# Performance work log

Hardware: AMD Instinct MI355X
Metric: run time of the kernel (lower is better)

Reference implementation:

```python
import jax, jax.numpy as jnp
import numpy as np

B, C_IN, W, H = 16, 512, 40, 40
HC = 64  # hide_channel


def setup_inputs() -> dict:
    key = jax.random.key(0)
    ks = jax.random.split(key, 6)
    def xavier(k, shape):
        fan_in, fan_out = shape
        lim = np.sqrt(6.0 / (fan_in + fan_out))
        return jax.random.uniform(k, shape, jnp.float32, -lim, lim)
    return {
        "rgb": jax.random.normal(ks[0], (B, C_IN, W, H), jnp.float32),
        "hsi": jax.random.normal(ks[1], (B, C_IN, W, H), jnp.float32),
        "wq": xavier(ks[2], (C_IN, HC)),
        "wk": xavier(ks[3], (C_IN, HC)),
        "wv": xavier(ks[4], (C_IN, HC)),
        "wo": xavier(ks[5], (HC, C_IN)),
    }


def reference(rgb, hsi, wq, wk, wv, wo):
    b, c, w, h = rgb.shape
    n = w * h
    # [B, C, W, H] -> [B, N, C] tokens
    x0 = jnp.swapaxes(rgb.reshape(b, c, n), 1, 2)
    x1 = jnp.swapaxes(hsi.reshape(b, c, n), 1, 2)
    q = x0 @ wq              # [B, N, HC]
    k = x0 @ wk              # [B, N, HC]
    v = x1 @ wv              # [B, N, HC]
    hc = q.shape[-1]
    scale = hc ** (-0.5)
    attn = jax.nn.softmax(jnp.einsum('bnd,bmd->bnm', q, k) * scale, axis=-1)  # [B, N, N]
    res = jnp.einsum('bnm,bmd->bnd', attn, v)  # [B, N, HC]
    # Faithful to torch: .transpose(1, 2).reshape(B, N, HC) (layout reinterpretation)
    res = jnp.swapaxes(res, 1, 2).reshape(b, n, hc)
    out = res @ wo                              # [B, N, C]
    out = jnp.swapaxes(out, 1, 2).reshape(b, c, w, h)
    return out
```

## Files before the change

### kernel.cpp

```cpp
#include <hip/hip_runtime.h>
#include <cstddef>

#define NB   16
#define CIN  512
#define NTOK 1600
#define HCH  64
#define LDA  72

typedef __attribute__((ext_vector_type(8))) short bf16x8;
typedef __attribute__((ext_vector_type(4))) float f32x4;

__device__ __forceinline__ unsigned short f2bf(float x) {
    union { float f; unsigned u; } v; v.f = x;
    unsigned r = v.u + 0x7FFFu + ((v.u >> 16) & 1u);
    return (unsigned short)(r >> 16);
}

__device__ __forceinline__ unsigned cvtpk_bf16(float lo, float hi) {
    unsigned r;
    asm("v_cvt_pk_bf16_f32 %0, %1, %2" : "=v"(r) : "v"(lo), "v"(hi));
    return r;
}

__device__ __forceinline__ float fast_exp2(float x) {
#if __has_builtin(__builtin_amdgcn_exp2f)
    return __builtin_amdgcn_exp2f(x);
#else
    return exp2f(x);
#endif
}

__global__ void __launch_bounds__(256) wprep_kernel(
    const float* __restrict__ wq, const float* __restrict__ wk,
    const float* __restrict__ wv, const float* __restrict__ wo,
    unsigned short* __restrict__ Wt, unsigned short* __restrict__ WoT)
{
    const int gid = blockIdx.x * 256 + threadIdx.x;
    if (gid < 3 * HCH * (CIN / 8)) {
        const int h  = gid & 63;
        const int c8 = (gid >> 6) & 63;
        const int t  = gid >> 12;
        const float* w = (t == 0) ? wq : (t == 1) ? wk : wv;
        ushort4 lo, hi;
        lo.x = f2bf(w[(size_t)(c8 * 8 + 0) * HCH + h]);
        lo.y = f2bf(w[(size_t)(c8 * 8 + 1) * HCH + h]);
        lo.z = f2bf(w[(size_t)(c8 * 8 + 2) * HCH + h]);
        lo.w = f2bf(w[(size_t)(c8 * 8 + 3) * HCH + h]);
        hi.x = f2bf(w[(size_t)(c8 * 8 + 4) * HCH + h]);
        hi.y = f2bf(w[(size_t)(c8 * 8 + 5) * HCH + h]);
        hi.z = f2bf(w[(size_t)(c8 * 8 + 6) * HCH + h]);
        hi.w = f2bf(w[(size_t)(c8 * 8 + 7) * HCH + h]);
        ushort4* dst = (ushort4*)(Wt + ((size_t)t * HCH + h) * CIN + c8 * 8);
        dst[0] = lo; dst[1] = hi;
    } else {
        const int g  = gid - 3 * HCH * (CIN / 8);
        const int c  = g & 511;
        const int j8 = g >> 9;
        ushort4 lo, hi;
        lo.x = f2bf(wo[(size_t)(j8 * 8 + 0) * CIN + c]);
        lo.y = f2bf(wo[(size_t)(j8 * 8 + 1) * CIN + c]);
        lo.z = f2bf(wo[(size_t)(j8 * 8 + 2) * CIN + c]);
        lo.w = f2bf(wo[(size_t)(j8 * 8 + 3) * CIN + c]);
        hi.x = f2bf(wo[(size_t)(j8 * 8 + 4) * CIN + c]);
        hi.y = f2bf(wo[(size_t)(j8 * 8 + 5) * CIN + c]);
        hi.z = f2bf(wo[(size_t)(j8 * 8 + 6) * CIN + c]);
        hi.w = f2bf(wo[(size_t)(j8 * 8 + 7) * CIN + c]);
        ushort4* dst = (ushort4*)(WoT + (size_t)c * HCH + j8 * 8);
        dst[0] = lo; dst[1] = hi;
    }
}

__global__ void __launch_bounds__(256) proj_kernel(
    const float* __restrict__ rgb, const float* __restrict__ hsi,
    const unsigned short* __restrict__ Wt,
    unsigned short* __restrict__ Q, unsigned short* __restrict__ K,
    unsigned short* __restrict__ Vt)
{
    __shared__ __align__(16) unsigned short As[64 * LDA];
    __shared__ __align__(16) unsigned short Ws[128 * LDA];

    const int which = blockIdx.y;
    const int b    = blockIdx.x / 25;
    const int n0   = (blockIdx.x % 25) * 64;
    const int tid  = threadIdx.x;
    const int wv_  = tid >> 6;
    const int lane = tid & 63;
    const int l16  = lane & 15, quad = lane >> 4;

    const float* __restrict__ src = which ? hsi : rgb;
    const unsigned short* __restrict__ wbase = Wt + (which ? (size_t)2 * HCH * CIN : 0);
    const int nW = which ? 1 : 2;

    f32x4 acc[2][4];
    #pragma unroll
    for (int t = 0; t < 2; ++t)
        #pragma unroll
        for (int nt = 0; nt < 4; ++nt)
            #pragma unroll
            for (int r = 0; r < 4; ++r) acc[t][nt][r] = 0.f;

    const int cc = tid >> 2;
    const int nq = tid & 3;
    const int swz = cc >> 3;
    const int clo = cc & 7;
    const int swzr = (l16 >> 1) & 6;

    for (int c0 = 0; c0 < CIN; c0 += 64) {
        __syncthreads();
        {
            const float* gs = src + ((size_t)b * CIN + c0 + cc) * NTOK + n0;
            #pragma unroll
            for (int rep = 0; rep < 4; ++rep) {
                const int nn4 = rep * 4 + nq;
                const float4 a = ((const float4*)gs)[nn4];
                const int n = nn4 * 4;
                const int i01 = ((swz ^ ((n >> 1) & 6)) << 3) + clo;
                const int i23 = ((swz ^ (((n + 2) >> 1) & 6)) << 3) + clo;
                As[(n + 0) * LDA + i01] = f2bf(a.x);
                As[(n + 1) * LDA + i01] = f2bf(a.y);
                As[(n + 2) * LDA + i23] = f2bf(a.z);
                As[(n + 3) * LDA + i23] = f2bf(a.w);
            }
        }
        for (int task = tid; task < nW * 512; task += 256) {
            const int row = task >> 3, ch = task & 7;
            *((int4*)(Ws + row * LDA + ch * 8)) =
                *((const int4*)(wbase + (size_t)row * CIN + c0 + ch * 8));
        }
        __syncthreads();

        #pragma unroll
        for (int k0 = 0; k0 < 2; ++k0) {
            const bf16x8 av = *((const bf16x8*)(As + (wv_ * 16 + l16) * LDA + ((k0 * 4 + quad) ^ swzr) * 8));
            if (which == 0) {
                #pragma unroll
                for (int t = 0; t < 2; ++t)
                    #pragma unroll
                    for (int nt = 0; nt < 4; ++nt) {
                        const bf16x8 bv = *((const bf16x8*)(Ws + (t * 64 + nt * 16 + l16) * LDA + k0 * 32 + quad * 8));
                        acc[t][nt] = __builtin_amdgcn_mfma_f32_16x16x32_bf16(av, bv, acc[t][nt], 0, 0, 0);
                    }
            } else {
                #pragma unroll
                for (int nt = 0; nt < 4; ++nt) {
                    const bf16x8 bv = *((const bf16x8*)(Ws + (nt * 16 + l16) * LDA + k0 * 32 + quad * 8));
                    acc[0][nt] = __builtin_amdgcn_mfma_f32_16x16x32_bf16(av, bv, acc[0][nt], 0, 0, 0);
                }
            }
        }
    }

    if (which == 0) {
        const float qscale = 0.18033688f;
        #pragma unroll
        for (int nt = 0; nt < 4; ++nt) {
            const int h = nt * 16 + l16;
            #pragma unroll
            for (int r = 0; r < 4; ++r) {
                const int n = n0 + wv_ * 16 + quad * 4 + r;
                Q[((size_t)b * NTOK + n) * HCH + h] = f2bf(acc[0][nt][r] * qscale);
                K[((size_t)b * NTOK + n) * HCH + h] = f2bf(acc[1][nt][r]);
            }
        }
    } else {
        const int pbase = n0 + (wv_ & 1) * 32 + quad * 8 + (wv_ >> 1) * 4;
        #pragma unroll
        for (int nt = 0; nt < 4; ++nt) {
            const int h = nt * 16 + l16;
            ushort4 pv;
            pv.x = f2bf(acc[0][nt][0]); pv.y = f2bf(acc[0][nt][1]);
            pv.z = f2bf(acc[0][nt][2]); pv.w = f2bf(acc[0][nt][3]);
            *((ushort4*)(Vt + ((size_t)b * HCH + h) * NTOK + pbase)) = pv;
        }
    }
}

__device__ __forceinline__ void attn_stage_tile(
    const unsigned short* __restrict__ Kg, const unsigned short* __restrict__ Vg,
    char* buf, int kt, int wv_, int srow, int scole)
{
    #pragma unroll
    for (int i = 0; i < 2; ++i) {
        const int ck  = i * 4 + wv_;
        const int row = ck * 8 + srow;
        const unsigned short* ksrc = Kg + (size_t)(kt * 64 + row) * HCH + scole;
        __builtin_amdgcn_global_load_lds(ksrc, buf + ck * 1024, 16, 0, 0);
        const unsigned short* vsrc = Vg + (size_t)row * NTOK + kt * 64 + scole;
        __builtin_amdgcn_global_load_lds(vsrc, buf + 8192 + ck * 1024, 16, 0, 0);
    }
}

__device__ __forceinline__ void attn_compute_lds(
    const char* kbuf, const char* vbuf, int l16, int quad,
    const bf16x8 (&qa)[2], f32x4 (&o)[4], float& rs)
{
    bf16x8 kb[2][4], vb[2][4];
    #pragma unroll
    for (int k0 = 0; k0 < 2; ++k0) {
        const int colb = (k0 * 64 + quad * 16) ^ ((l16 & 7) << 4);
        #pragma unroll
        for (int nt = 0; nt < 4; ++nt) {
            kb[k0][nt] = *((const bf16x8*)(kbuf + (nt * 16 + l16) * 128 + colb));
            vb[k0][nt] = *((const bf16x8*)(vbuf + (nt * 16 + l16) * 128 + colb));
        }
    }

    f32x4 s[4];
    #pragma unroll
    for (int nt = 0; nt < 4; ++nt)
        #pragma unroll
        for (int r = 0; r < 4; ++r) s[nt][r] = 0.f;
    #pragma unroll
    for (int k0 = 0; k0 < 2; ++k0)
        #pragma unroll
        for (int nt = 0; nt < 4; ++nt)
            s[nt] = __builtin_amdgcn_mfma_f32_16x16x32_bf16(kb[k0][nt], qa[k0], s[nt], 0, 0, 0);

    unsigned dA[4], dB[4];
    #pragma unroll
    for (int nt = 0; nt < 4; ++nt) {
        const float e0 = fast_exp2(s[nt][0]);
        const float e1 = fast_exp2(s[nt][1]);
        const float e2 = fast_exp2(s[nt][2]);
        const float e3 = fast_exp2(s[nt][3]);
        rs += (e0 + e1) + (e2 + e3);
        dA[nt] = cvtpk_bf16(e0, e1);
        dB[nt] = cvtpk_bf16(e2, e3);
    }

    #pragma unroll
    for (int k0 = 0; k0 < 2; ++k0) {
        union { bf16x8 v; unsigned u[4]; } pu;
        pu.u[0] = dA[k0];
        pu.u[1] = dB[k0];
        pu.u[2] = dA[k0 + 2];
        pu.u[3] = dB[k0 + 2];
        #pragma unroll
        for (int nt = 0; nt < 4; ++nt)
            o[nt] = __builtin_amdgcn_mfma_f32_16x16x32_bf16(pu.v, vb[k0][nt], o[nt], 0, 0, 0);
    }
}

__global__ void __launch_bounds__(256) attn_kernel(
    const unsigned short* __restrict__ Q, const unsigned short* __restrict__ K,
    const unsigned short* __restrict__ Vt, unsigned short* __restrict__ Rt2)
{
    __shared__ __align__(16) char sbuf[2][16384];

    const int bx   = blockIdx.x;
    const int b    = 2 * (bx & 7) + (((bx >> 3) >= 25) ? 1 : 0);
    const int qt   = (bx >> 3) % 25;
    const int tid  = threadIdx.x;
    const int wv_  = tid >> 6;
    const int lane = tid & 63;
    const int l16  = lane & 15, quad = lane >> 4;

    const unsigned short* Qg = Q  + ((size_t)b * NTOK + qt * 64 + wv_ * 16) * HCH;
    const unsigned short* Kg = K  + (size_t)b * NTOK * HCH;
    const unsigned short* Vg = Vt + (size_t)b * HCH * NTOK;

    const int srow  = lane >> 3;
    const int scole = 8 * ((lane & 7) ^ srow);

    bf16x8 qa[2];
    #pragma unroll
    for (int k0 = 0; k0 < 2; ++k0)
        qa[k0] = *((const bf16x8*)(Qg + (size_t)l16 * HCH + k0 * 32 + quad * 8));

    f32x4 o[4];
    float rs = 0.f;
    #pragma unroll
    for (int nt = 0; nt < 4; ++nt)
        #pragma unroll
        for (int r = 0; r < 4; ++r) o[nt][r] = 0.f;

    attn_stage_tile(Kg, Vg, sbuf[0], 0, wv_, srow, scole);
    int cur = 0;
    for (int kt = 0; kt < 25; ++kt) {
        if (kt + 1 < 25) {
            attn_stage_tile(Kg, Vg, sbuf[cur ^ 1], kt + 1, wv_, srow, scole);
            asm volatile("s_waitcnt vmcnt(4)" ::: "memory");
        } else {
            asm volatile("s_waitcnt vmcnt(0)" ::: "memory");
        }
        __builtin_amdgcn_sched_barrier(0);
        __builtin_amdgcn_s_barrier();
        __builtin_amdgcn_sched_barrier(0);
        attn_compute_lds(sbuf[cur], sbuf[cur] + 8192, l16, quad, qa, o, rs);
        __builtin_amdgcn_sched_barrier(0);
        __builtin_amdgcn_s_barrier();
        cur ^= 1;
    }

    rs += __shfl_xor(rs, 16);
    rs += __shfl_xor(rs, 32);
    float rsq[4];
    #pragma unroll
    for (int r = 0; r < 4; ++r) rsq[r] = __shfl(rs, quad * 4 + r);

    unsigned short* Rg = Rt2 + ((size_t)(b * 25 + qt)) * HCH * HCH;
    #pragma unroll
    for (int nt = 0; nt < 4; ++nt) {
        ushort4 pk;
        pk.x = f2bf(o[nt][0] / rsq[0]);
        pk.y = f2bf(o[nt][1] / rsq[1]);
        pk.z = f2bf(o[nt][2] / rsq[2]);
        pk.w = f2bf(o[nt][3] / rsq[3]);
        *((ushort4*)(Rg + (size_t)(nt * 16 + l16) * HCH + wv_ * 16 + quad * 4)) = pk;
    }
}

__global__ void __launch_bounds__(256) outproj_kernel(
    const unsigned short* __restrict__ Rt2, const unsigned short* __restrict__ WoT,
    float* __restrict__ out)
{
    __shared__ __align__(16) unsigned short Aw[64 * LDA];

    const int b    = blockIdx.x;
    const int ct   = blockIdx.y;
    const int nt64 = blockIdx.z;
    const int tid  = threadIdx.x;
    const int wv_  = tid >> 6;
    const int lane = tid & 63;
    const int l16  = lane & 15, quad = lane >> 4;

    #pragma unroll
    for (int r = 0; r < 2; ++r) {
        const int task = tid + r * 256;
        const int row = task >> 3, ch = task & 7;
        *((int4*)(Aw + row * LDA + ch * 8)) =
            *((const int4*)(WoT + ((size_t)(ct * 64 + row)) * HCH + ch * 8));
    }
    __syncthreads();

    const int n = nt64 * 64 + wv_ * 16 + l16;
    const int h = n / 25, t = n % 25;
    const unsigned short* bsrc = Rt2 + ((size_t)(b * 25 + t) * HCH + h) * HCH;

    f32x4 acc[4];
    #pragma unroll
    for (int mt = 0; mt < 4; ++mt)
        #pragma unroll
        for (int r = 0; r < 4; ++r) acc[mt][r] = 0.f;

    #pragma unroll
    for (int k0 = 0; k0 < 2; ++k0) {
        const bf16x8 bv = *((const bf16x8*)(bsrc + k0 * 32 + quad * 8));
        #pragma unroll
        for (int mt = 0; mt < 4; ++mt) {
            const bf16x8 av = *((const bf16x8*)(Aw + (mt * 16 + l16) * LDA + k0 * 32 + quad * 8));
            acc[mt] = __builtin_amdgcn_mfma_f32_16x16x32_bf16(av, bv, acc[mt], 0, 0, 0);
        }
    }
    #pragma unroll
    for (int mt = 0; mt < 4; ++mt)
        #pragma unroll
        for (int r = 0; r < 4; ++r)
            out[((size_t)b * CIN + ct * 64 + mt * 16 + quad * 4 + r) * NTOK + n] = acc[mt][r];
}

extern "C" void kernel_launch(void* const* d_in, const int* in_sizes, int n_in,
                              void* d_out, int out_size, void* d_ws, size_t ws_size,
                              hipStream_t stream)
{
    const float* rgb = (const float*)d_in[0];
    const float* hsi = (const float*)d_in[1];
    const float* wq  = (const float*)d_in[2];
    const float* wk  = (const float*)d_in[3];
    const float* wv  = (const float*)d_in[4];
    const float* wo  = (const float*)d_in[5];
    float* out = (float*)d_out;

    unsigned short* Wt  = (unsigned short*)d_ws;
    unsigned short* WoT = Wt  + (size_t)3 * HCH * CIN;
    unsigned short* Qb  = WoT + (size_t)CIN * HCH;
    unsigned short* Kb  = Qb  + (size_t)NB * NTOK * HCH;
    unsigned short* Vtb = Kb  + (size_t)NB * NTOK * HCH;
    unsigned short* Rt2 = Vtb + (size_t)NB * NTOK * HCH;

    wprep_kernel<<<dim3(64), 256, 0, stream>>>(wq, wk, wv, wo, Wt, WoT);
    proj_kernel<<<dim3(NB * 25, 2), 256, 0, stream>>>(rgb, hsi, Wt, Qb, Kb, Vtb);
    attn_kernel<<<dim3(NB * 25), 256, 0, stream>>>(Qb, Kb, Vtb, Rt2);
    outproj_kernel<<<dim3(NB, 8, 25), 256, 0, stream>>>(Rt2, WoT, out);
}
```

Baseline: 184.6 us.

## Double-buffer projection kernel with async LDS weight DMA and register prefetch

The projection GEMM now double-buffers its activation and weight LDS tiles. The next fp32 input chunk is prefetched into registers, and weights are loaded directly into LDS with global_load_lds using an XOR swizzle. Hand-placed waitcnt and barrier calls overlap these loads with MFMA compute on the current chunk, replacing the old load-sync-compute loop. Templating on the weight count removes the runtime branch, at the cost of doubled LDS use and fragile manual vmcnt accounting.

```diff
diff --git a/kernel.cpp b/kernel.cpp
--- a/kernel.cpp
+++ b/kernel.cpp
@@ -70,87 +70,134 @@
     }
 }
 
-__global__ void __launch_bounds__(256) proj_kernel(
-    const float* __restrict__ rgb, const float* __restrict__ hsi,
-    const unsigned short* __restrict__ Wt,
+__device__ __forceinline__ void proj_load_in(
+    const float* __restrict__ gsb, int c0, int nq, float4 (&inr)[4])
+{
+    #pragma unroll
+    for (int rep = 0; rep < 4; ++rep)
+        inr[rep] = ((const float4*)(gsb + (size_t)c0 * NTOK))[rep * 4 + nq];
+}
+
+__device__ __forceinline__ void proj_write_as(
+    unsigned short* Ab, const float4 (&inr)[4], int nq, int swz, int clo)
+{
+    #pragma unroll
+    for (int rep = 0; rep < 4; ++rep) {
+        const int nn4 = rep * 4 + nq;
+        const float4 a = inr[rep];
+        const int n = nn4 * 4;
+        const int i01 = ((swz ^ ((n >> 1) & 6)) << 3) + clo;
+        const int i23 = ((swz ^ (((n + 2) >> 1) & 6)) << 3) + clo;
+        Ab[(n + 0) * LDA + i01] = f2bf(a.x);
+        Ab[(n + 1) * LDA + i01] = f2bf(a.y);
+        Ab[(n + 2) * LDA + i23] = f2bf(a.z);
+        Ab[(n + 3) * LDA + i23] = f2bf(a.w);
+    }
+}
+
+template<int NW>
+__device__ __forceinline__ void proj_dma_w(
+    const unsigned short* __restrict__ wbase, int c0,
+    unsigned short* Wb, int wv_, int lane)
+{
+    const int sr = lane >> 3;
+    const int sc = 8 * ((lane & 7) ^ sr);
+    #pragma unroll
+    for (int r = 0; r < 2 * NW; ++r) {
+        const int row0 = r * 32 + wv_ * 8;
+        __builtin_amdgcn_global_load_lds(
+            wbase + (size_t)(row0 + sr) * CIN + c0 + sc,
+            (char*)Wb + row0 * 128, 16, 0, 0);
+    }
+}
+
+template<int NW>
+__device__ __forceinline__ void proj_compute(
+    const unsigned short* Ab, const unsigned short* Wb,
+    int wv_, int l16, int quad, int swzr, f32x4 (&acc)[NW][4])
+{
+    #pragma unroll
+    for (int k0 = 0; k0 < 2; ++k0) {
+        const bf16x8 av = *((const bf16x8*)(Ab + (wv_ * 16 + l16) * LDA + ((k0 * 4 + quad) ^ swzr) * 8));
+        const int colb = (k0 * 64 + quad * 16) ^ ((l16 & 7) << 4);
+        #pragma unroll
+        for (int t = 0; t < NW; ++t)
+            #pragma unroll
+            for (int nt = 0; nt < 4; ++nt) {
+                const bf16x8 bv = *((const bf16x8*)((const char*)Wb + (t * 64 + nt * 16 + l16) * 128 + colb));
+                acc[t][nt] = __builtin_amdgcn_mfma_f32_16x16x32_bf16(av, bv, acc[t][nt], 0, 0, 0);
+            }
+    }
+}
+
+template<int NW>
+__device__ __forceinline__ void proj_body(
+    const float* __restrict__ src, const unsigned short* __restrict__ wbase,
     unsigned short* __restrict__ Q, unsigned short* __restrict__ K,
-    unsigned short* __restrict__ Vt)
-{
-    __shared__ __align__(16) unsigned short As[64 * LDA];
-    __shared__ __align__(16) unsigned short Ws[128 * LDA];
-
-    const int which = blockIdx.y;
-    const int b    = blockIdx.x / 25;
-    const int n0   = (blockIdx.x % 25) * 64;
-    const int tid  = threadIdx.x;
+    unsigned short* __restrict__ Vt,
+    unsigned short* As, unsigned short* Wl, int b, int n0, int tid)
+{
     const int wv_  = tid >> 6;
     const int lane = tid & 63;
     const int l16  = lane & 15, quad = lane >> 4;
-
-    const float* __restrict__ src = which ? hsi : rgb;
-    const unsigned short* __restrict__ wbase = Wt + (which ? (size_t)2 * HCH * CIN : 0);
-    const int nW = which ? 1 : 2;
-
-    f32x4 acc[2][4];
-    #pragma unroll
-    for (int t = 0; t < 2; ++t)
+    const int cc   = tid >> 2, nq = tid & 3;
+    const int swz  = cc >> 3,  clo = cc & 7;
+    const int swzr = (l16 >> 1) & 6;
+
+    f32x4 acc[NW][4];
+    #pragma unroll
+    for (int t = 0; t < NW; ++t)
         #pragma unroll
         for (int nt = 0; nt < 4; ++nt)
             #pragma unroll
             for (int r = 0; r < 4; ++r) acc[t][nt][r] = 0.f;
 
-    const int cc = tid >> 2;
-    const int nq = tid & 3;
-    const int swz = cc >> 3;
-    const int clo = cc & 7;
-    const int swzr = (l16 >> 1) & 6;
-
-    for (int c0 = 0; c0 < CIN; c0 += 64) {
-        __syncthreads();
-        {
-            const float* gs = src + ((size_t)b * CIN + c0 + cc) * NTOK + n0;
-            #pragma unroll
-            for (int rep = 0; rep < 4; ++rep) {
-                const int nn4 = rep * 4 + nq;
-                const float4 a = ((const float4*)gs)[nn4];
-                const int n = nn4 * 4;
-                const int i01 = ((swz ^ ((n >> 1) & 6)) << 3) + clo;
-                const int i23 = ((swz ^ (((n + 2) >> 1) & 6)) << 3) + clo;
-                As[(n + 0) * LDA + i01] = f2bf(a.x);
-                As[(n + 1) * LDA + i01] = f2bf(a.y);
-                As[(n + 2) * LDA + i23] = f2bf(a.z);
-                As[(n + 3) * LDA + i23] = f2bf(a.w);
+    const float* gsb = src + ((size_t)b * CIN + cc) * NTOK + n0;
+
+    float4 inr[4];
+    proj_load_in(gsb, 0, nq, inr);
+    __builtin_amdgcn_sched_barrier(0);
+    proj_dma_w<NW>(wbase, 0, Wl, wv_, lane);
+    if constexpr (NW == 2) asm volatile("s_waitcnt vmcnt(4)" ::: "memory");
+    else                   asm volatile("s_waitcnt vmcnt(2)" ::: "memory");
+    __builtin_amdgcn_sched_barrier(0);
+    proj_write_as(As, inr, nq, swz, clo);
+    proj_load_in(gsb, 64, nq, inr);
+    __builtin_amdgcn_sched_barrier(0);
+    proj_dma_w<NW>(wbase, 64, Wl + 128 * 64, wv_, lane);
+    if constexpr (NW == 2) asm volatile("s_waitcnt vmcnt(8) lgkmcnt(0)" ::: "memory");
+    else                   asm volatile("s_waitcnt vmcnt(6) lgkmcnt(0)" ::: "memory");
+    __builtin_amdgcn_sched_barrier(0);
+    __builtin_amdgcn_s_barrier();
+    __builtin_amdgcn_sched_barrier(0);
+
+    for (int t = 0; t < 8; ++t) {
+        proj_compute<NW>(As + (t & 1) * (64 * LDA), Wl + (t & 1) * (128 * 64),
+                         wv_, l16, quad, swzr, acc);
+        __builtin_amdgcn_sched_barrier(0);
+        __builtin_amdgcn_s_barrier();
+        __builtin_amdgcn_sched_barrier(0);
+        if (t < 7) {
+            if constexpr (NW == 2) asm volatile("s_waitcnt vmcnt(4)" ::: "memory");
+            else                   asm volatile("s_waitcnt vmcnt(2)" ::: "memory");
+            __builtin_amdgcn_sched_barrier(0);
+            proj_write_as(As + ((t + 1) & 1) * (64 * LDA), inr, nq, swz, clo);
+            if (t < 6) {
+                proj_load_in(gsb, (t + 2) * 64, nq, inr);
+                __builtin_amdgcn_sched_barrier(0);
+                proj_dma_w<NW>(wbase, (t + 2) * 64, Wl + (t & 1) * (128 * 64), wv_, lane);
+                if constexpr (NW == 2) asm volatile("s_waitcnt vmcnt(8) lgkmcnt(0)" ::: "memory");
+                else                   asm volatile("s_waitcnt vmcnt(6) lgkmcnt(0)" ::: "memory");
+            } else {
+                asm volatile("s_waitcnt vmcnt(0) lgkmcnt(0)" ::: "memory");
             }
-        }
-        for (int task = tid; task < nW * 512; task += 256) {
-            const int row = task >> 3, ch = task & 7;
-            *((int4*)(Ws + row * LDA + ch * 8)) =
-                *((const int4*)(wbase + (size_t)row * CIN + c0 + ch * 8));
-        }
-        __syncthreads();
-
-        #pragma unroll
-        for (int k0 = 0; k0 < 2; ++k0) {
-            const bf16x8 av = *((const bf16x8*)(As + (wv_ * 16 + l16) * LDA + ((k0 * 4 + quad) ^ swzr) * 8));
-            if (which == 0) {
-                #pragma unroll
-                for (int t = 0; t < 2; ++t)
-                    #pragma unroll
-                    for (int nt = 0; nt < 4; ++nt) {
-                        const bf16x8 bv = *((const bf16x8*)(Ws + (t * 64 + nt * 16 + l16) * LDA + k0 * 32 + quad * 8));
-                        acc[t][nt] = __builtin_amdgcn_mfma_f32_16x16x32_bf16(av, bv, acc[t][nt], 0, 0, 0);
-                    }
-            } else {
-                #pragma unroll
-                for (int nt = 0; nt < 4; ++nt) {
-                    const bf16x8 bv = *((const bf16x8*)(Ws + (nt * 16 + l16) * LDA + k0 * 32 + quad * 8));
-                    acc[0][nt] = __builtin_amdgcn_mfma_f32_16x16x32_bf16(av, bv, acc[0][nt], 0, 0, 0);
-                }
-            }
-        }
-    }
-
-    if (which == 0) {
+            __builtin_amdgcn_sched_barrier(0);
+            __builtin_amdgcn_s_barrier();
+            __builtin_amdgcn_sched_barrier(0);
+        }
+    }
+
+    if constexpr (NW == 2) {
         const float qscale = 0.18033688f;
         #pragma unroll
         for (int nt = 0; nt < 4; ++nt) {
@@ -175,6 +222,26 @@
     }
 }
 
+__global__ void __launch_bounds__(256) proj_kernel(
+    const float* __restrict__ rgb, const float* __restrict__ hsi,
+    const unsigned short* __restrict__ Wt,
+    unsigned short* __restrict__ Q, unsigned short* __restrict__ K,
+    unsigned short* __restrict__ Vt)
+{
+    __shared__ __align__(16) unsigned short As[2 * 64 * LDA];
+    __shared__ __align__(16) unsigned short Wl[2 * 128 * 64];
+
+    const int which = blockIdx.y;
+    const int b     = blockIdx.x / 25;
+    const int n0    = (blockIdx.x % 25) * 64;
+    const unsigned short* wbase = Wt + (which ? (size_t)2 * HCH * CIN : 0);
+
+    if (which == 0)
+        proj_body<2>(rgb, wbase, Q, K, Vt, As, Wl, b, n0, threadIdx.x);
+    else
+        proj_body<1>(hsi, wbase, Q, K, Vt, As, Wl, b, n0, threadIdx.x);
+}
+
 __device__ __forceinline__ void attn_stage_tile(
     const unsigned short* __restrict__ Kg, const unsigned short* __restrict__ Vg,
     char* buf, int kt, int wv_, int srow, int scole)
```

Measured after the change: 186.0 us. About the same (+0.7%).

## Restructure projection kernel with full-weight LDS preload and register-pipelined input loads

Applied to the files above, without the earlier changes.

The projection kernel now loads the whole 64x512 bf16 weight slice into LDS once, using global_load_lds with an XOR swizzle. Input channels are streamed through per-wave 16-row strips, with two register buffers in flight so global loads overlap the bf16 conversion and MFMA work. Block-wide syncs inside the channel loop are dropped. The grid grows from 2 to 3 in y so Q and K get separate blocks, which means the rgb input is read twice instead of once in exchange for fewer accumulators and more parallelism.

```diff
diff --git a/kernel.cpp b/kernel.cpp
--- a/kernel.cpp
+++ b/kernel.cpp
@@ -70,14 +70,52 @@
     }
 }
 
+__device__ __forceinline__ void proj_ld(
+    const float* __restrict__ gsb, int c0, float4 (&r)[4])
+{
+    #pragma unroll
+    for (int e = 0; e < 2; ++e)
+        #pragma unroll
+        for (int f4 = 0; f4 < 2; ++f4)
+            r[e * 2 + f4] = ((const float4*)(gsb + (size_t)(c0 + e) * NTOK))[f4];
+}
+
+__device__ __forceinline__ void proj_wr(
+    unsigned short* strip, const float4 (&r)[4], int cp, int to)
+{
+    const float* a0 = (const float*)&r[0];
+    const float* a1 = (const float*)&r[2];
+    #pragma unroll
+    for (int j = 0; j < 8; ++j) {
+        const unsigned pk = cvtpk_bf16(a0[j], a1[j]);
+        *((unsigned*)(strip + (to * 8 + j) * LDA + 2 * cp)) = pk;
+    }
+}
+
+__device__ __forceinline__ void proj_mm(
+    const unsigned short* strip, const unsigned short* Ws,
+    int t8, int l16, int quad, f32x4 (&acc)[4])
+{
+    #pragma unroll
+    for (int k0 = 0; k0 < 2; ++k0) {
+        const bf16x8 av = *((const bf16x8*)(strip + l16 * LDA + k0 * 32 + quad * 8));
+        const int chunk = t8 * 8 + ((k0 * 4 + quad) ^ (l16 & 7));
+        #pragma unroll
+        for (int nt = 0; nt < 4; ++nt) {
+            const bf16x8 bv = *((const bf16x8*)((const char*)Ws + (nt * 16 + l16) * 1024 + chunk * 16));
+            acc[nt] = __builtin_amdgcn_mfma_f32_16x16x32_bf16(av, bv, acc[nt], 0, 0, 0);
+        }
+    }
+}
+
 __global__ void __launch_bounds__(256) proj_kernel(
     const float* __restrict__ rgb, const float* __restrict__ hsi,
     const unsigned short* __restrict__ Wt,
     unsigned short* __restrict__ Q, unsigned short* __restrict__ K,
     unsigned short* __restrict__ Vt)
 {
-    __shared__ __align__(16) unsigned short As[64 * LDA];
-    __shared__ __align__(16) unsigned short Ws[128 * LDA];
+    __shared__ __align__(16) unsigned short Ws[64 * 512];
+    __shared__ __align__(16) unsigned short strips[4][16 * LDA];
 
     const int which = blockIdx.y;
     const int b    = blockIdx.x / 25;
@@ -87,67 +125,46 @@
     const int lane = tid & 63;
     const int l16  = lane & 15, quad = lane >> 4;
 
-    const float* __restrict__ src = which ? hsi : rgb;
-    const unsigned short* __restrict__ wbase = Wt + (which ? (size_t)2 * HCH * CIN : 0);
-    const int nW = which ? 1 : 2;
-
-    f32x4 acc[2][4];
-    #pragma unroll
-    for (int t = 0; t < 2; ++t)
-        #pragma unroll
-        for (int nt = 0; nt < 4; ++nt)
-            #pragma unroll
-            for (int r = 0; r < 4; ++r) acc[t][nt][r] = 0.f;
-
-    const int cc = tid >> 2;
-    const int nq = tid & 3;
-    const int swz = cc >> 3;
-    const int clo = cc & 7;
-    const int swzr = (l16 >> 1) & 6;
-
-    for (int c0 = 0; c0 < CIN; c0 += 64) {
-        __syncthreads();
-        {
-            const float* gs = src + ((size_t)b * CIN + c0 + cc) * NTOK + n0;
-            #pragma unroll
-            for (int rep = 0; rep < 4; ++rep) {
-                const int nn4 = rep * 4 + nq;
-                const float4 a = ((const float4*)gs)[nn4];
-                const int n = nn4 * 4;
-                const int i01 = ((swz ^ ((n >> 1) & 6)) << 3) + clo;
-                const int i23 = ((swz ^ (((n + 2) >> 1) & 6)) << 3) + clo;
-                As[(n + 0) * LDA + i01] = f2bf(a.x);
-                As[(n + 1) * LDA + i01] = f2bf(a.y);
-                As[(n + 2) * LDA + i23] = f2bf(a.z);
-                As[(n + 3) * LDA + i23] = f2bf(a.w);
-            }
-        }
-        for (int task = tid; task < nW * 512; task += 256) {
-            const int row = task >> 3, ch = task & 7;
-            *((int4*)(Ws + row * LDA + ch * 8)) =
-                *((const int4*)(wbase + (size_t)row * CIN + c0 + ch * 8));
-        }
-        __syncthreads();
-
-        #pragma unroll
-        for (int k0 = 0; k0 < 2; ++k0) {
-            const bf16x8 av = *((const bf16x8*)(As + (wv_ * 16 + l16) * LDA + ((k0 * 4 + quad) ^ swzr) * 8));
-            if (which == 0) {
-                #pragma unroll
-                for (int t = 0; t < 2; ++t)
-                    #pragma unroll
-                    for (int nt = 0; nt < 4; ++nt) {
-                        const bf16x8 bv = *((const bf16x8*)(Ws + (t * 64 + nt * 16 + l16) * LDA + k0 * 32 + quad * 8));
-                        acc[t][nt] = __builtin_amdgcn_mfma_f32_16x16x32_bf16(av, bv, acc[t][nt], 0, 0, 0);
-                    }
-            } else {
-                #pragma unroll
-                for (int nt = 0; nt < 4; ++nt) {
-                    const bf16x8 bv = *((const bf16x8*)(Ws + (nt * 16 + l16) * LDA + k0 * 32 + quad * 8));
-                    acc[0][nt] = __builtin_amdgcn_mfma_f32_16x16x32_bf16(av, bv, acc[0][nt], 0, 0, 0);
-                }
-            }
-        }
+    const float* __restrict__ src = (which == 2) ? hsi : rgb;
+    const unsigned short* __restrict__ wbase = Wt + (size_t)which * HCH * CIN;
+
+    {
+        const int scg = (lane >> 3) * 64;
+        #pragma unroll
+        for (int i = 0; i < 16; ++i) {
+            const int row = wv_ * 16 + i;
+            const unsigned short* s = wbase + (size_t)row * CIN
+                                      + scg + 8 * ((lane & 7) ^ (row & 7));
+            __builtin_amdgcn_global_load_lds(s, (char*)Ws + row * 1024, 16, 0, 0);
+        }
+    }
+
+    const int cp = lane & 31;
+    const int to = lane >> 5;
+    const float* gsb = src + ((size_t)b * CIN + 2 * cp) * NTOK + n0 + wv_ * 16 + to * 8;
+    unsigned short* strip = strips[wv_];
+
+    float4 inr[2][4];
+    proj_ld(gsb, 0, inr[0]);
+    proj_ld(gsb, 64, inr[1]);
+    asm volatile("s_waitcnt vmcnt(8)" ::: "memory");
+    __builtin_amdgcn_sched_barrier(0);
+    __builtin_amdgcn_s_barrier();
+
+    f32x4 acc[4];
+    #pragma unroll
+    for (int nt = 0; nt < 4; ++nt)
+        #pragma unroll
+        for (int r = 0; r < 4; ++r) acc[nt][r] = 0.f;
+
+    #pragma unroll
+    for (int t = 0; t < 8; ++t) {
+        if (t < 7) asm volatile("s_waitcnt vmcnt(4)" ::: "memory");
+        else       asm volatile("s_waitcnt vmcnt(0)" ::: "memory");
+        __builtin_amdgcn_sched_barrier(0);
+        proj_wr(strip, inr[t & 1], cp, to);
+        if (t + 2 < 8) proj_ld(gsb, (t + 2) * 64, inr[t & 1]);
+        proj_mm(strip, Ws, t, l16, quad, acc);
     }
 
     if (which == 0) {
@@ -158,8 +175,17 @@
             #pragma unroll
             for (int r = 0; r < 4; ++r) {
                 const int n = n0 + wv_ * 16 + quad * 4 + r;
-                Q[((size_t)b * NTOK + n) * HCH + h] = f2bf(acc[0][nt][r] * qscale);
-                K[((size_t)b * NTOK + n) * HCH + h] = f2bf(acc[1][nt][r]);
+                Q[((size_t)b * NTOK + n) * HCH + h] = f2bf(acc[nt][r] * qscale);
+            }
+        }
+    } else if (which == 1) {
+        #pragma unroll
+        for (int nt = 0; nt < 4; ++nt) {
+            const int h = nt * 16 + l16;
+            #pragma unroll
+            for (int r = 0; r < 4; ++r) {
+                const int n = n0 + wv_ * 16 + quad * 4 + r;
+                K[((size_t)b * NTOK + n) * HCH + h] = f2bf(acc[nt][r]);
             }
         }
     } else {
@@ -168,8 +194,8 @@
         for (int nt = 0; nt < 4; ++nt) {
             const int h = nt * 16 + l16;
             ushort4 pv;
-            pv.x = f2bf(acc[0][nt][0]); pv.y = f2bf(acc[0][nt][1]);
-            pv.z = f2bf(acc[0][nt][2]); pv.w = f2bf(acc[0][nt][3]);
+            pv.x = f2bf(acc[nt][0]); pv.y = f2bf(acc[nt][1]);
+            pv.z = f2bf(acc[nt][2]); pv.w = f2bf(acc[nt][3]);
             *((ushort4*)(Vt + ((size_t)b * HCH + h) * NTOK + pbase)) = pv;
         }
     }
@@ -379,7 +405,7 @@
     unsigned short* Rt2 = Vtb + (size_t)NB * NTOK * HCH;
 
     wprep_kernel<<<dim3(64), 256, 0, stream>>>(wq, wk, wv, wo, Wt, WoT);
-    proj_kernel<<<dim3(NB * 25, 2), 256, 0, stream>>>(rgb, hsi, Wt, Qb, Kb, Vtb);
+    proj_kernel<<<dim3(NB * 25, 3), 256, 0, stream>>>(rgb, hsi, Wt, Qb, Kb, Vtb);
     attn_kernel<<<dim3(NB * 25), 256, 0, stream>>>(Qb, Kb, Vtb, Rt2);
     outproj_kernel<<<dim3(NB, 8, 25), 256, 0, stream>>>(Rt2, WoT, out);
 }
```

After: 190.2 us. 1.03x slower.
